# Optimization experiments

Measured on AMD Instinct MI355X. Metric: run time of the kernel, lower is better.

The kernel has to match this reference:

```python
import jax, jax.numpy as jnp
import numpy as np

# ---- module constants (from init_kwargs) ----
N_DIM = 2                      # n: latent dim (len(active_dims))
T_STEPS = 100                  # t: linspace(0,1,t) integration grid
M_PER_DIM = 12                 # m = [12,12] HSGP basis per dim
C_FACTOR = 1.5                 # c: HSGP domain expansion factor
X_EXTENT = 3.0                 # data extent (x0 ~ N(0,1) lives in [-3,3])
L_BOUND = C_FACTOR * X_EXTENT  # HSGP half-domain length L = c*S
D_COMPS = N_DIM * (N_DIM + 1) // 2  # d = 3 metric components

# eigen-index grid over all dim combinations: [M_TOTAL, n]
_J = np.stack(np.meshgrid(*[np.arange(1, M_PER_DIM + 1)] * N_DIM, indexing='ij'), -1)
J = jnp.asarray(_J.reshape(-1, N_DIM).astype(np.float32))
M_TOTAL = J.shape[0]
_r, _c = np.triu_indices(N_DIM)
ROWS, COLS = jnp.asarray(_r), jnp.asarray(_c)

# explicit Adams-Bashforth coefficients (orders 1..4), newest derivative first
AB_COEFFS = jnp.array([
    [1.0, 0.0, 0.0, 0.0],
    [1.5, -0.5, 0.0, 0.0],
    [23.0/12.0, -16.0/12.0, 5.0/12.0, 0.0],
    [55.0/24.0, -59.0/24.0, 37.0/24.0, -9.0/24.0]], dtype=jnp.float32)


def hsgp_features(x, ls, alpha):
    """HSGP ExpQuad linearized basis phi(x) and its spatial derivative dphi.
    x: [B, n] -> phi: [B, M], dphi: [B, M, n]."""
    w = jnp.pi * J / (2.0 * L_BOUND)                  # [M, n] per-dim frequencies
    arg = w[None] * (x[:, None, :] + L_BOUND)         # [B, M, n]
    s, c = jnp.sin(arg), jnp.cos(arg)
    norm = L_BOUND ** (-0.5 * N_DIM)
    phi = norm * jnp.prod(s, axis=-1)                 # [B, M]
    dcols = []
    for i in range(N_DIM):                            # structural loop over n=2 dims
        p = w[None, :, i] * c[:, :, i]
        for j2 in range(N_DIM):
            if j2 != i:
                p = p * s[:, :, j2]
        dcols.append(norm * p)
    dphi = jnp.stack(dcols, axis=-1)                  # [B, M, n]
    # ExpQuad spectral density sqrt weights
    S = (alpha ** 2) * ((2.0 * jnp.pi) ** (0.5 * N_DIM)) * jnp.prod(ls) \
        * jnp.exp(-0.5 * jnp.sum((ls ** 2)[None] * w ** 2, axis=-1))  # [M]
    sq = jnp.sqrt(S)
    return phi * sq[None], dphi * sq[None, :, None]


def geodesic_rhs(y, beta, ls, alpha):
    """geomstats-style geodesic equation: y = stack([x, v]) -> stack([v, a]),
    a^k = -Gamma^k_{ij} v^i v^j with GP-parameterized Christoffels."""
    x, v = y[0], y[1]                                 # [B, n]
    B = x.shape[0]
    phi, dphi = hsgp_features(x, ls, alpha)
    f = phi @ beta.T                                  # [B, d] metric components
    df = jnp.einsum('bmi,dm->bdi', dphi, beta)        # [B, d, n] their derivatives
    G = jnp.zeros((B, N_DIM, N_DIM), x.dtype)
    G = G.at[:, ROWS, COLS].set(f).at[:, COLS, ROWS].set(f)
    G = G + jnp.eye(N_DIM, dtype=x.dtype)             # identity offset keeps G invertible
    D = jnp.zeros((B, N_DIM, N_DIM, N_DIM), x.dtype)  # D[b,l,j,i] = d_i g_{lj}
    D = D.at[:, ROWS, COLS, :].set(df).at[:, COLS, ROWS, :].set(df)
    Ginv = jnp.linalg.inv(G)
    # term[b,l,i,j] = d_i g_{lj} + d_j g_{li} - d_l g_{ij}
    term = jnp.transpose(D, (0, 1, 3, 2)) + D - jnp.transpose(D, (0, 3, 1, 2))
    Gam = 0.5 * jnp.einsum('bkl,blij->bkij', Ginv, term)
    acc = -jnp.einsum('bkij,bi,bj->bk', Gam, v, v)
    return jnp.stack([v, acc])


def adams_integrate(y0, beta, ls, alpha, rhs):
    """Fixed-grid explicit Adams (order<=4, lower-order startup) over linspace(0,1,t)."""
    h = jnp.float32(1.0 / (T_STEPS - 1))
    hist0 = jnp.zeros((4,) + y0.shape, y0.dtype)
    def step(carry, idx):
        y, hist = carry
        fcur = rhs(y, beta, ls, alpha)
        hist = jnp.concatenate([fcur[None], hist[:-1]], axis=0)  # newest first
        coef = AB_COEFFS[jnp.minimum(idx, 3)]
        y_next = y + h * jnp.tensordot(coef, hist, axes=1)
        return (y_next, hist), y_next
    _, ys = jax.lax.scan(step, (y0, hist0), jnp.arange(T_STEPS - 1))
    return jnp.concatenate([y0[None], ys], axis=0)    # [t, 2, B, n]


def setup_inputs():
    key = jax.random.key(0)
    k1, k2, k3, k4 = jax.random.split(key, 4)
    B = 50000
    x0 = jax.random.normal(k1, (B, N_DIM), jnp.float32)
    v0 = 0.2 * jax.random.normal(k2, (B, N_DIM), jnp.float32)
    beta = 0.05 * jax.random.normal(k3, (D_COMPS, M_TOTAL), jnp.float32)
    ls = 0.3 + 0.5 * jax.random.uniform(k4, (N_DIM,), jnp.float32)
    alpha = jnp.float32(1.0)
    return {"x0": x0, "v0": v0, "beta": beta, "ls": ls, "alpha": alpha}


def reference(x0, v0, beta, ls, alpha):
    y0 = jnp.stack([x0, v0])                          # [2, B, n]
    return adams_integrate(y0, beta, ls, alpha, geodesic_rhs)
```

## Files before the change

### kernel.cpp

```cpp
#include <hip/hip_runtime.h>
#include <math.h>

typedef _Float16 h4 __attribute__((ext_vector_type(4)));
typedef _Float16 h2 __attribute__((ext_vector_type(2)));
typedef float    f4 __attribute__((ext_vector_type(4)));

namespace {
constexpr float LB = 4.5f;
constexpr float WF = (float)M_PI / (2.0f * LB);
constexpr float REV = 1.0f / (4.0f * LB);
}

__global__ void setup_A_kernel(const float* __restrict__ beta,
                               const float* __restrict__ ls,
                               const float* __restrict__ alpha,
                               _Float16* __restrict__ A) {
    int idx = blockIdx.x * blockDim.x + threadIdx.x;
    if (idx >= 1792) return;
    int d2 = idx >> 8;
    int l = (idx >> 2) & 63;
    int t = idx & 3;
    int r = l & 15;
    int k = ((l >> 4) << 2) + t;
    float val = 0.0f;
    if (d2 == 6) {
        val = ((k & 3) == (r & 3)) ? 1.0f : 0.0f;
    } else if (r < 12 && k < 12) {
        int d = (d2 >= 3) ? d2 - 3 : d2;
        float w0 = WF * (float)(r + 1);
        float w1 = WF * (float)(k + 1);
        float l0 = ls[0], l1 = ls[1], al = alpha[0];
        float S = al * al * (2.0f * (float)M_PI) * l0 * l1 *
                  expf(-0.5f * (l0 * l0 * w0 * w0 + l1 * l1 * w1 * w1));
        val = beta[d * 144 + r * 12 + k] * sqrtf(S) * (1.0f / LB);
        if (d2 >= 3) val *= WF * (float)(k + 1);
    }
    A[idx] = (_Float16)val;
}

__device__ __forceinline__ void trig4r(float thr, float mb, float* s, float* c) {
    float s1 = __builtin_amdgcn_sinf(thr);
    float c1 = __builtin_amdgcn_cosf(thr);
    float mbr = mb * thr;
    s[0] = __builtin_amdgcn_sinf(mbr);
    c[0] = __builtin_amdgcn_cosf(mbr);
    #pragma unroll
    for (int t = 1; t < 4; ++t) {
        s[t] = fmaf(s[t - 1], c1,  c[t - 1] * s1);
        c[t] = fmaf(c[t - 1], c1, -(s[t - 1] * s1));
    }
}

__device__ __forceinline__ h4 pack4(float a, float b, float c, float d) {
    h2 lo = __builtin_bit_cast(h2, __builtin_amdgcn_cvt_pkrtz(a, b));
    h2 hi = __builtin_bit_cast(h2, __builtin_amdgcn_cvt_pkrtz(c, d));
    return __builtin_shufflevector(lo, hi, 0, 1, 2, 3);
}

__global__ __launch_bounds__(64)
void geo_kernel(const float* __restrict__ xg, const float* __restrict__ vg,
                const _Float16* Ag ,
                float* __restrict__ out, int B)
{
    int lane = threadIdx.x;
    int ebase = blockIdx.x << 4;
    if (ebase >= B) return;
    int g = lane >> 4;
    int e = ebase + (lane & 15);
    if (e >= B) e = B - 1;

    union U8 { uint2 u; h4 h; };
    const uint2* Au = reinterpret_cast<const uint2*>(Ag);
    U8 a0, a1, a2, a3, a4, a5, a6;
    a0.u = Au[0 * 64 + lane];
    a1.u = Au[1 * 64 + lane];
    a2.u = Au[2 * 64 + lane];
    a3.u = Au[3 * 64 + lane];
    a4.u = Au[4 * 64 + lane];
    a5.u = Au[5 * 64 + lane];
    a6.u = Au[6 * 64 + lane];
    asm volatile("" ::: "memory");
    h4 A0 = a0.h, A1 = a1.h, A2 = a2.h;
    h4 A3 = a3.h, A4 = a4.h, A5 = a5.h;
    h4 SEL = a6.h;

    float mb = (float)(4 * g + 1);
    float Wm[4];
    #pragma unroll
    for (int t = 0; t < 4; ++t) Wm[t] = WF * (mb + (float)t);

    float2 xv = reinterpret_cast<const float2*>(xg)[e];
    float2 vv2 = reinterpret_cast<const float2*>(vg)[e];
    float x0 = xv.x, x1 = xv.y, v0 = vv2.x, v1 = vv2.y;

    unsigned off = 4u * ((((unsigned)(g >> 1) * (unsigned)B) + (unsigned)e) * 2u
                         + (unsigned)(g & 1));
    const unsigned stride = 16u * (unsigned)B;
    char* outc = reinterpret_cast<char*>(out);
    {
        float sval = (g & 2) ? ((g & 1) ? v1 : v0) : ((g & 1) ? x1 : x0);
        *reinterpret_cast<float*>(outc + off) = sval;
    }

    float h1x = 0.f, h2x = 0.f, h3x = 0.f, h1y = 0.f, h2y = 0.f, h3y = 0.f;
    float g1x = 0.f, g2x = 0.f, g3x = 0.f, g1y = 0.f, g2y = 0.f, g3y = 0.f;
    const float h = 1.0f / 99.0f;

    auto STEP = [&](float hc0, float hc1, float hc2, float hc3) {
        float s0v[4], c0v[4], s1v[4], c1v[4], wc0[4];
        trig4r(fmaf(x0, REV, LB * REV), mb, s0v, c0v);
        trig4r(fmaf(x1, REV, LB * REV), mb, s1v, c1v);
        #pragma unroll
        for (int t = 0; t < 4; ++t) wc0[t] = Wm[t] * c0v[t];

        h4 bs = pack4(s1v[0], s1v[1], s1v[2], s1v[3]);
        h4 bc = pack4(c1v[0], c1v[1], c1v[2], c1v[3]);

        f4 z = {0.f, 0.f, 0.f, 0.f};
        f4 u0 = __builtin_amdgcn_mfma_f32_16x16x16f16(A0, bs, z, 0, 0, 0);
        f4 u1 = __builtin_amdgcn_mfma_f32_16x16x16f16(A1, bs, z, 0, 0, 0);
        f4 u2 = __builtin_amdgcn_mfma_f32_16x16x16f16(A2, bs, z, 0, 0, 0);
        f4 w0 = __builtin_amdgcn_mfma_f32_16x16x16f16(A3, bc, z, 0, 0, 0);
        f4 w1 = __builtin_amdgcn_mfma_f32_16x16x16f16(A4, bc, z, 0, 0, 0);
        f4 w2 = __builtin_amdgcn_mfma_f32_16x16x16f16(A5, bc, z, 0, 0, 0);

        float f0 = 0.f, f1 = 0.f, f2 = 0.f;
        float dA0 = 0.f, dA1 = 0.f, dA2 = 0.f;
        float dB0 = 0.f, dB1 = 0.f, dB2 = 0.f;
        #pragma unroll
        for (int t = 0; t < 4; ++t) {
            float sA = s0v[t], cA = wc0[t];
            f0  = fmaf(sA, u0[t], f0);   dA0 = fmaf(cA, u0[t], dA0);
            f1  = fmaf(sA, u1[t], f1);   dA1 = fmaf(cA, u1[t], dA1);
            f2  = fmaf(sA, u2[t], f2);   dA2 = fmaf(cA, u2[t], dA2);
            dB0 = fmaf(sA, w0[t], dB0);
            dB1 = fmaf(sA, w1[t], dB1);
            dB2 = fmaf(sA, w2[t], dB2);
        }

        float vv00 = v0 * v0, vv11 = v1 * v1;
        float w01 = 2.0f * v0 * v1;
        float q0p = fmaf(dA0, vv00, fmaf(dB0, w01, fmaf(2.0f, dB1, -dA2) * vv11));
        float q1p = fmaf(fmaf(2.0f, dA1, -dB0), vv00, fmaf(dA2, w01, dB2 * vv11));

        h4 r1 = pack4(f0, f1, f2, q0p);
        h4 r2 = pack4(q1p, 0.0f, 0.0f, 0.0f);
        f4 D1 = __builtin_amdgcn_mfma_f32_16x16x16f16(SEL, r1, z, 0, 0, 0);
        f4 D2 = __builtin_amdgcn_mfma_f32_16x16x16f16(SEL, r2, z, 0, 0, 0);
        float F0 = D1[0], F1 = D1[1], F2 = D1[2], Q0 = D1[3], Q1 = D2[0];

        float G00 = F0 + 1.0f, G01 = F1, G11 = F2 + 1.0f;
        float det = fmaf(G00, G11, -(G01 * G01));
        float rdet = __builtin_amdgcn_rcpf(det);
        float a0v = -0.5f * rdet * fmaf(G11, Q0, -(G01 * Q1));
        float a1v = -0.5f * rdet * fmaf(G00, Q1, -(G01 * Q0));

        x0 = fmaf(hc0, v0, fmaf(hc1, h1x, fmaf(hc2, h2x, fmaf(hc3, h3x, x0))));
        x1 = fmaf(hc0, v1, fmaf(hc1, h1y, fmaf(hc2, h2y, fmaf(hc3, h3y, x1))));
        float nv0 = fmaf(hc0, a0v, fmaf(hc1, g1x, fmaf(hc2, g2x, fmaf(hc3, g3x, v0))));
        float nv1 = fmaf(hc0, a1v, fmaf(hc1, g1y, fmaf(hc2, g2y, fmaf(hc3, g3y, v1))));
        h3x = h2x; h2x = h1x; h1x = v0;  h3y = h2y; h2y = h1y; h1y = v1;
        g3x = g2x; g2x = g1x; g1x = a0v; g3y = g2y; g2y = g1y; g1y = a1v;
        v0 = nv0; v1 = nv1;

        off += stride;
        float sval = (g & 2) ? ((g & 1) ? v1 : v0) : ((g & 1) ? x1 : x0);
        *reinterpret_cast<float*>(outc + off) = sval;
    };

    STEP(h * 1.0f, 0.0f, 0.0f, 0.0f);
    STEP(h * 1.5f, h * -0.5f, 0.0f, 0.0f);
    STEP(h * 23.0f / 12.0f, h * -16.0f / 12.0f, h * 5.0f / 12.0f, 0.0f);
    #pragma unroll 4
    for (int t = 3; t < 99; ++t)
        STEP(h * 55.0f / 24.0f, h * -59.0f / 24.0f, h * 37.0f / 24.0f, h * -9.0f / 24.0f);
}

extern "C" void kernel_launch(void* const* d_in, const int* in_sizes, int n_in,
                              void* d_out, int out_size, void* d_ws, size_t ws_size,
                              hipStream_t stream) {
    const float* x0    = (const float*)d_in[0];
    const float* v0    = (const float*)d_in[1];
    const float* beta  = (const float*)d_in[2];
    const float* ls    = (const float*)d_in[3];
    const float* alpha = (const float*)d_in[4];
    float* out = (float*)d_out;
    _Float16* A = (_Float16*)d_ws;

    int B = in_sizes[0] / 2;

    hipLaunchKernelGGL(setup_A_kernel, dim3(28), dim3(64), 0, stream,
                       beta, ls, alpha, A);

    int grid = (B + 15) / 16;
    hipLaunchKernelGGL(geo_kernel, dim3(grid), dim3(64), 0, stream,
                       x0, v0, A, out, B);
}
```

Baseline: 122.8 us.

## Software-pipeline geodesic step: compute next position's basis MFMAs before current acceleration

Position x for the next step depends only on v and history, so it is updated first. The trig and basis MFMA front end for that next position is then issued while the current step's metric solve and selection MFMAs run, which breaks the serial dependency chain within each step. The goal is to hide MFMA and transcendental latency under low occupancy (64-thread blocks). In exchange it needs more live registers, and the unroll factor drops from 4 to 2 with a peeled final step.

```diff
diff --git a/kernel.cpp b/kernel.cpp
--- a/kernel.cpp
+++ b/kernel.cpp
@@ -106,10 +106,15 @@
     float g1x = 0.f, g2x = 0.f, g3x = 0.f, g1y = 0.f, g2y = 0.f, g3y = 0.f;
     const float h = 1.0f / 99.0f;
 
-    auto STEP = [&](float hc0, float hc1, float hc2, float hc3) {
+    float pf0, pf1, pf2, pA0, pA1, pA2, pB0, pB1, pB2;
+
+    auto FRONT = [&](float xa, float xb,
+                     float& f0, float& f1, float& f2,
+                     float& dA0, float& dA1, float& dA2,
+                     float& dB0, float& dB1, float& dB2) {
         float s0v[4], c0v[4], s1v[4], c1v[4], wc0[4];
-        trig4r(fmaf(x0, REV, LB * REV), mb, s0v, c0v);
-        trig4r(fmaf(x1, REV, LB * REV), mb, s1v, c1v);
+        trig4r(fmaf(xa, REV, 0.25f), mb, s0v, c0v);
+        trig4r(fmaf(xb, REV, 0.25f), mb, s1v, c1v);
         #pragma unroll
         for (int t = 0; t < 4; ++t) wc0[t] = Wm[t] * c0v[t];
 
@@ -124,9 +129,9 @@
         f4 w1 = __builtin_amdgcn_mfma_f32_16x16x16f16(A4, bc, z, 0, 0, 0);
         f4 w2 = __builtin_amdgcn_mfma_f32_16x16x16f16(A5, bc, z, 0, 0, 0);
 
-        float f0 = 0.f, f1 = 0.f, f2 = 0.f;
-        float dA0 = 0.f, dA1 = 0.f, dA2 = 0.f;
-        float dB0 = 0.f, dB1 = 0.f, dB2 = 0.f;
+        f0 = 0.f; f1 = 0.f; f2 = 0.f;
+        dA0 = 0.f; dA1 = 0.f; dA2 = 0.f;
+        dB0 = 0.f; dB1 = 0.f; dB2 = 0.f;
         #pragma unroll
         for (int t = 0; t < 4; ++t) {
             float sA = s0v[t], cA = wc0[t];
@@ -137,14 +142,28 @@
             dB1 = fmaf(sA, w1[t], dB1);
             dB2 = fmaf(sA, w2[t], dB2);
         }
+    };
+
+    FRONT(x0, x1, pf0, pf1, pf2, pA0, pA1, pA2, pB0, pB1, pB2);
+
+    auto STEP = [&](float hc0, float hc1, float hc2, float hc3, bool front) {
+        float nx0 = fmaf(hc0, v0, fmaf(hc1, h1x, fmaf(hc2, h2x, fmaf(hc3, h3x, x0))));
+        float nx1 = fmaf(hc0, v1, fmaf(hc1, h1y, fmaf(hc2, h2y, fmaf(hc3, h3y, x1))));
+        h3x = h2x; h2x = h1x; h1x = v0;
+        h3y = h2y; h2y = h1y; h1y = v1;
+
+        float nf0, nf1, nf2, nA0, nA1, nA2, nB0, nB1, nB2;
+        if (front)
+            FRONT(nx0, nx1, nf0, nf1, nf2, nA0, nA1, nA2, nB0, nB1, nB2);
 
         float vv00 = v0 * v0, vv11 = v1 * v1;
         float w01 = 2.0f * v0 * v1;
-        float q0p = fmaf(dA0, vv00, fmaf(dB0, w01, fmaf(2.0f, dB1, -dA2) * vv11));
-        float q1p = fmaf(fmaf(2.0f, dA1, -dB0), vv00, fmaf(dA2, w01, dB2 * vv11));
-
-        h4 r1 = pack4(f0, f1, f2, q0p);
+        float q0p = fmaf(pA0, vv00, fmaf(pB0, w01, fmaf(2.0f, pB1, -pA2) * vv11));
+        float q1p = fmaf(fmaf(2.0f, pA1, -pB0), vv00, fmaf(pA2, w01, pB2 * vv11));
+
+        h4 r1 = pack4(pf0, pf1, pf2, q0p);
         h4 r2 = pack4(q1p, 0.0f, 0.0f, 0.0f);
+        f4 z = {0.f, 0.f, 0.f, 0.f};
         f4 D1 = __builtin_amdgcn_mfma_f32_16x16x16f16(SEL, r1, z, 0, 0, 0);
         f4 D2 = __builtin_amdgcn_mfma_f32_16x16x16f16(SEL, r2, z, 0, 0, 0);
         float F0 = D1[0], F1 = D1[1], F2 = D1[2], Q0 = D1[3], Q1 = D2[0];
@@ -155,25 +174,30 @@
         float a0v = -0.5f * rdet * fmaf(G11, Q0, -(G01 * Q1));
         float a1v = -0.5f * rdet * fmaf(G00, Q1, -(G01 * Q0));
 
-        x0 = fmaf(hc0, v0, fmaf(hc1, h1x, fmaf(hc2, h2x, fmaf(hc3, h3x, x0))));
-        x1 = fmaf(hc0, v1, fmaf(hc1, h1y, fmaf(hc2, h2y, fmaf(hc3, h3y, x1))));
         float nv0 = fmaf(hc0, a0v, fmaf(hc1, g1x, fmaf(hc2, g2x, fmaf(hc3, g3x, v0))));
         float nv1 = fmaf(hc0, a1v, fmaf(hc1, g1y, fmaf(hc2, g2y, fmaf(hc3, g3y, v1))));
-        h3x = h2x; h2x = h1x; h1x = v0;  h3y = h2y; h2y = h1y; h1y = v1;
-        g3x = g2x; g2x = g1x; g1x = a0v; g3y = g2y; g2y = g1y; g1y = a1v;
-        v0 = nv0; v1 = nv1;
+        g3x = g2x; g2x = g1x; g1x = a0v;
+        g3y = g2y; g2y = g1y; g1y = a1v;
+
+        x0 = nx0; x1 = nx1; v0 = nv0; v1 = nv1;
+        if (front) {
+            pf0 = nf0; pf1 = nf1; pf2 = nf2;
+            pA0 = nA0; pA1 = nA1; pA2 = nA2;
+            pB0 = nB0; pB1 = nB1; pB2 = nB2;
+        }
 
         off += stride;
         float sval = (g & 2) ? ((g & 1) ? v1 : v0) : ((g & 1) ? x1 : x0);
         *reinterpret_cast<float*>(outc + off) = sval;
     };
 
-    STEP(h * 1.0f, 0.0f, 0.0f, 0.0f);
-    STEP(h * 1.5f, h * -0.5f, 0.0f, 0.0f);
-    STEP(h * 23.0f / 12.0f, h * -16.0f / 12.0f, h * 5.0f / 12.0f, 0.0f);
-    #pragma unroll 4
-    for (int t = 3; t < 99; ++t)
-        STEP(h * 55.0f / 24.0f, h * -59.0f / 24.0f, h * 37.0f / 24.0f, h * -9.0f / 24.0f);
+    STEP(h * 1.0f, 0.0f, 0.0f, 0.0f, true);
+    STEP(h * 1.5f, h * -0.5f, 0.0f, 0.0f, true);
+    STEP(h * 23.0f / 12.0f, h * -16.0f / 12.0f, h * 5.0f / 12.0f, 0.0f, true);
+    #pragma unroll 2
+    for (int t = 3; t < 98; ++t)
+        STEP(h * 55.0f / 24.0f, h * -59.0f / 24.0f, h * 37.0f / 24.0f, h * -9.0f / 24.0f, true);
+    STEP(h * 55.0f / 24.0f, h * -59.0f / 24.0f, h * 37.0f / 24.0f, h * -9.0f / 24.0f, false);
 }
 
 extern "C" void kernel_launch(void* const* d_in, const int* in_sizes, int n_in,
```

After: 116.3 us, median of 2. 1.06x faster.
